# Performance work log

Hardware: AMD Instinct MI355X
Metric: run time of the kernel (lower is better)

## Reference

```python
import jax, jax.numpy as jnp
import numpy as np

B, L, H = 2, 4096, 1024


def _rope_tables(seq_len, dim, base=10000.0):
    # standard RoPE cos/sin tables, rotate-half convention, shape [L, dim]
    inv_freq = 1.0 / (base ** (np.arange(0, dim, 2, dtype=np.float32) / dim))
    t = np.arange(seq_len, dtype=np.float32)
    freqs = np.outer(t, inv_freq)                      # [L, dim/2]
    emb = np.concatenate([freqs, freqs], axis=-1)      # [L, dim]
    return jnp.asarray(np.cos(emb)), jnp.asarray(np.sin(emb))


def setup_inputs() -> dict:
    key = jax.random.key(0)
    k1, k2 = jax.random.split(key)
    hidden_states = jax.random.normal(k1, (B, L, H), dtype=jnp.float32)
    # queries weight: normal with std = initializer_range / sqrt(2*num_layers*hidden)
    std = 0.02 / np.sqrt(2.0 * 24 * H)
    W_q = jax.random.normal(k2, (H, H), dtype=jnp.float32) * std
    cos, sin = _rope_tables(L, H)
    return {"hidden_states": hidden_states, "W_q": W_q, "cos": cos, "sin": sin}


def _rotate_half(x):
    x1, x2 = jnp.split(x, 2, axis=-1)
    return jnp.concatenate([-x2, x1], axis=-1)


def reference(hidden_states, W_q, cos, sin):
    # dropout with p=0.0 (eval) -> identity
    h = hidden_states * cos[None, :, :] + _rotate_half(hidden_states) * sin[None, :, :]  # RoPE, [B,L,H]
    q = jnp.einsum('blh,oh->blo', h, W_q)          # F.linear(h, W_q), [B,L,H]
    pre_attn = jnp.einsum('blh,bmh->blm', q, h)    # Q @ K^T (no softmax), [B,L,L]
    attention = jnp.einsum('blm,bmh->blh', pre_attn, h)  # scores @ V, [B,L,H]
    return attention
```

## Files before the change

### kernel.cpp

```cpp
#include <hip/hip_runtime.h>
#include <hip/hip_bf16.h>
#include <stdint.h>

#define BB 2
#define LL 4096
#define HH 1024
#define GBK 32

typedef __bf16 bf16;
typedef __bf16 bf16x4 __attribute__((ext_vector_type(4)));
typedef __bf16 bf16x8 __attribute__((ext_vector_type(8)));
typedef float  f32x4  __attribute__((ext_vector_type(4)));

__device__ __forceinline__ void async_cp16(const bf16* g, const bf16* l)
{
    typedef const uint32_t __attribute__((address_space(1)))* gp_t;
    typedef uint32_t __attribute__((address_space(3)))* lp_t;
    __builtin_amdgcn_global_load_lds((gp_t)(uintptr_t)g, (lp_t)(uintptr_t)l, 16, 0, 0);
}

__device__ __forceinline__ uint32_t pack_bf16(float lo, float hi)
{
    union { bf16 b; unsigned short u; } a, c;
    a.b = (bf16)lo; c.b = (bf16)hi;
    return (uint32_t)a.u | ((uint32_t)c.u << 16);
}

__global__ __launch_bounds__(256) void prep_kernel(
    const float* __restrict__ x, const float* __restrict__ cs,
    const float* __restrict__ sn, const float* __restrict__ Wq,
    bf16* __restrict__ h, bf16* __restrict__ hT, bf16* __restrict__ Wb)
{
    const int id = blockIdx.x;
    if (id >= 1024) {
        const long base = (long)(id - 1024) * 4096 + (long)threadIdx.x * 16;
#pragma unroll
        for (int j = 0; j < 4; ++j) {
            const float4 v = *(const float4*)(Wq + base + j * 4);
            bf16x4 o;
            o[0] = (bf16)v.x; o[1] = (bf16)v.y; o[2] = (bf16)v.z; o[3] = (bf16)v.w;
            *(bf16x4*)(Wb + base + j * 4) = o;
        }
        return;
    }
    __shared__ uint32_t lds[2][64][36];
    const int b  = id >> 9;
    const int v  = id & 511;
    const int r0 = (v >> 3) * 64;
    const int c0 = (v & 7) * 64;
    const int t  = threadIdx.x;
    const int c8 = t & 7;
    const int rr = t >> 3;
    const int ca = c0 + c8 * 8;
    const long xrow0 = ((long)b * LL + r0 + 2 * rr) * HH;
    const long crow0 = (long)(r0 + 2 * rr) * HH;

    float oA[2][8], oB[2][8];
#pragma unroll
    for (int rw = 0; rw < 2; ++rw) {
        const long xr = xrow0 + (long)rw * HH;
        const long cr = crow0 + (long)rw * HH;
        float xA[8], xB[8], cA[8], sA[8];
        *(float4*)&xA[0] = *(const float4*)(x + xr + ca);
        *(float4*)&xA[4] = *(const float4*)(x + xr + ca + 4);
        *(float4*)&xB[0] = *(const float4*)(x + xr + ca + 512);
        *(float4*)&xB[4] = *(const float4*)(x + xr + ca + 516);
        *(float4*)&cA[0] = *(const float4*)(cs + cr + ca);
        *(float4*)&cA[4] = *(const float4*)(cs + cr + ca + 4);
        *(float4*)&sA[0] = *(const float4*)(sn + cr + ca);
        *(float4*)&sA[4] = *(const float4*)(sn + cr + ca + 4);
#pragma unroll
        for (int j = 0; j < 8; ++j) {
            oA[rw][j] = xA[j] * cA[j] - xB[j] * sA[j];
            oB[rw][j] = xB[j] * cA[j] + xA[j] * sA[j];
        }
        bf16x8 hA, hB;
#pragma unroll
        for (int j = 0; j < 8; ++j) { hA[j] = (bf16)oA[rw][j]; hB[j] = (bf16)oB[rw][j]; }
        *(bf16x8*)(h + xr + ca)       = hA;
        *(bf16x8*)(h + xr + ca + 512) = hB;
    }
#pragma unroll
    for (int j = 0; j < 8; ++j) {
        lds[0][c8 * 8 + j][rr] = pack_bf16(oA[0][j], oA[1][j]);
        lds[1][c8 * 8 + j][rr] = pack_bf16(oB[0][j], oB[1][j]);
    }
    __syncthreads();

    const int cc = t >> 2;
    const int q  = t & 3;
#pragma unroll
    for (int s = 0; s < 2; ++s) {
        const int hrow = (s ? c0 + 512 : c0) + cc;
        bf16* po = hT + (long)b * HH * LL + (long)hrow * LL + r0 + q * 16;
        const uint4 w0 = *(const uint4*)&lds[s][cc][q * 8];
        const uint4 w1 = *(const uint4*)&lds[s][cc][q * 8 + 4];
        *(uint4*)(po)     = w0;
        *(uint4*)(po + 8) = w1;
    }
}

__global__ __launch_bounds__(128) void rope_kernel(
    const float* __restrict__ x, const float* __restrict__ cs,
    const float* __restrict__ sn, bf16* __restrict__ h)
{
    const int l = blockIdx.x;
    const int b = blockIdx.y;
    const int i = threadIdx.x * 4;
    const long xb = ((long)b * LL + l) * HH;
    const long cb = (long)l * HH;
    const float4 x1 = *(const float4*)(x + xb + i);
    const float4 x2 = *(const float4*)(x + xb + i + HH / 2);
    const float4 c1 = *(const float4*)(cs + cb + i);
    const float4 c2 = *(const float4*)(cs + cb + i + HH / 2);
    const float4 s1 = *(const float4*)(sn + cb + i);
    const float4 s2 = *(const float4*)(sn + cb + i + HH / 2);
    bf16x4 o1, o2;
    o1[0] = (bf16)(x1.x * c1.x - x2.x * s1.x);
    o1[1] = (bf16)(x1.y * c1.y - x2.y * s1.y);
    o1[2] = (bf16)(x1.z * c1.z - x2.z * s1.z);
    o1[3] = (bf16)(x1.w * c1.w - x2.w * s1.w);
    o2[0] = (bf16)(x2.x * c2.x + x1.x * s2.x);
    o2[1] = (bf16)(x2.y * c2.y + x1.y * s2.y);
    o2[2] = (bf16)(x2.z * c2.z + x1.z * s2.z);
    o2[3] = (bf16)(x2.w * c2.w + x1.w * s2.w);
    *(bf16x4*)(h + xb + i)          = o1;
    *(bf16x4*)(h + xb + i + HH / 2) = o2;
}

__global__ __launch_bounds__(256) void transpose_bf16_64(
    const bf16* __restrict__ in, bf16* __restrict__ out, const int R, const int C)
{
    __shared__ uint32_t lds[64][36];
    const long zoff = (long)blockIdx.z * R * C;
    const int r0 = blockIdx.x * 64;
    const int c0 = blockIdx.y * 64;
    const int t  = threadIdx.x;
    const int c8 = t & 7;
    const int rr = t >> 3;
    const bf16* p0 = in + zoff + (long)(r0 + 2 * rr) * C + c0 + c8 * 8;
    const uint4 ra = *(const uint4*)p0;
    const uint4 rb = *(const uint4*)(p0 + C);
    const uint32_t av[4] = {ra.x, ra.y, ra.z, ra.w};
    const uint32_t bv[4] = {rb.x, rb.y, rb.z, rb.w};
#pragma unroll
    for (int j = 0; j < 4; ++j) {
        const uint32_t alo = av[j] & 0xffffu, ahi = av[j] >> 16;
        const uint32_t blo = bv[j] & 0xffffu, bhi = bv[j] >> 16;
        lds[c8 * 8 + 2 * j    ][rr] = alo | (blo << 16);
        lds[c8 * 8 + 2 * j + 1][rr] = ahi | (bhi << 16);
    }
    __syncthreads();
    const int c = t >> 2;
    const int q = t & 3;
    const uint4 w0 = *(const uint4*)&lds[c][q * 8];
    const uint4 w1 = *(const uint4*)&lds[c][q * 8 + 4];
    bf16* po = out + zoff + (long)(c0 + c) * R + r0 + q * 16;
    *(uint4*)(po)     = w0;
    *(uint4*)(po + 8) = w1;
}

__global__ __launch_bounds__(256) void cast_wq(
    const float* __restrict__ Wq, bf16* __restrict__ Wb)
{
    const long idx = ((long)blockIdx.x * 256 + threadIdx.x) * 4;
    const float4 v = *(const float4*)(Wq + idx);
    bf16x4 o;
    o[0] = (bf16)v.x; o[1] = (bf16)v.y; o[2] = (bf16)v.z; o[3] = (bf16)v.w;
    *(bf16x4*)(Wb + idx) = o;
}

#define GEMM_SHARED()                                                          \
    __shared__ __align__(16) bf16 As_[2][128][32];                             \
    __shared__ __align__(16) bf16 Bs_[2][128][32];

#define GEMM_PREFETCH(KOFF, BUF)                                               \
    do {                                                                       \
        async_cp16(Ag + (KOFF),           &As_[BUF][0][0] + woff0);            \
        async_cp16(Ag + (KOFF) + 64L * K, &As_[BUF][0][0] + woff1);            \
        async_cp16(Bg + (KOFF),           &Bs_[BUF][0][0] + woff0);            \
        async_cp16(Bg + (KOFF) + 64L * K, &Bs_[BUF][0][0] + woff1);            \
    } while (0)

#define GEMM_BODY(M0, N0, KBASE, KEND, DST, DT, LDN)                           \
    {                                                                          \
        const int tid  = threadIdx.x;                                          \
        const int lane = tid & 63;                                             \
        const int wave = tid >> 6;                                             \
        const int wm = (wave & 1) * 64;                                        \
        const int wn = (wave >> 1) * 64;                                       \
        const int fr = lane & 15;                                              \
        const int fq = lane >> 4;                                              \
        const int srow = tid >> 2;                                             \
        const int scol = (tid & 3) * 8;                                        \
        const int woff0 = wave * 512;                                          \
        const int woff1 = 2048 + wave * 512;                                   \
        const bf16* Ag = Ab + (long)((M0) + srow) * K + scol;                  \
        const bf16* Bg = Bb + (long)((N0) + srow) * K + scol;                  \
        const f32x4 vzero = {0.f, 0.f, 0.f, 0.f};                              \
        f32x4 acc[4][4];                                                       \
        _Pragma("unroll") for (int i = 0; i < 4; ++i)                          \
            _Pragma("unroll") for (int j = 0; j < 4; ++j) acc[i][j] = vzero;   \
        GEMM_PREFETCH(KBASE, 0);                                               \
        int buf = 0;                                                           \
        for (int k0 = (KBASE); k0 < (KEND); k0 += GBK, buf ^= 1) {             \
            __syncthreads();                                                   \
            if (k0 + GBK < (KEND)) GEMM_PREFETCH(k0 + GBK, buf ^ 1);           \
            bf16x8 af[4], bfv[4];                                              \
            _Pragma("unroll") for (int i = 0; i < 4; ++i)                      \
                af[i]  = *(const bf16x8*)&As_[buf][wm + i * 16 + fr][fq * 8];  \
            _Pragma("unroll") for (int j = 0; j < 4; ++j)                      \
                bfv[j] = *(const bf16x8*)&Bs_[buf][wn + j * 16 + fr][fq * 8];  \
            _Pragma("unroll") for (int i = 0; i < 4; ++i)                      \
                _Pragma("unroll") for (int j = 0; j < 4; ++j)                  \
                    acc[i][j] = __builtin_amdgcn_mfma_f32_16x16x32_bf16(       \
                        af[i], bfv[j], acc[i][j], 0, 0, 0);                    \
        }                                                                      \
        _Pragma("unroll") for (int i = 0; i < 4; ++i) {                        \
            _Pragma("unroll") for (int r = 0; r < 4; ++r) {                    \
                const int row = (M0) + wm + i * 16 + fq * 4 + r;               \
                _Pragma("unroll") for (int j = 0; j < 4; ++j) {                \
                    const int col = (N0) + wn + j * 16 + fr;                   \
                    (DST)[(long)row * (LDN) + col] = (DT)acc[i][j][r];         \
                }                                                              \
            }                                                                  \
        }                                                                      \
    }

template <typename OUT_T>
__global__ __launch_bounds__(256) void gemm_bt(
    const bf16* __restrict__ A, const bf16* __restrict__ B, OUT_T* __restrict__ C,
    const int M, const int N, const int K,
    const long sA, const long sB, const long sC)
{
    GEMM_SHARED();
    const bf16* Ab = A + blockIdx.z * sA;
    const bf16* Bb = B + blockIdx.z * sB;
    OUT_T*      Cb = C + blockIdx.z * sC;
    const int m0 = blockIdx.x * 128;
    const int n0 = blockIdx.y * 128;
    GEMM_BODY(m0, n0, 0, K, Cb, OUT_T, N);
}

#define E_STAGE_A(KT, PART, BUF)                                               \
  do {                                                                         \
    const int kk0_ = kbase + (KT) * 64;                                        \
    _Pragma("unroll") for (int qq_ = 0; qq_ < 2; ++qq_) {                      \
      const int ch_  = qq_ * 512 + tid;                                        \
      const int sl_  = ch_ >> 3;                                               \
      const int cc_  = (ch_ & 7) ^ (sl_ & 7);                                  \
      const int row_ = (sl_ & 63) + (PART) * 64 + ((sl_ >> 6) << 7);           \
      async_cp16(Ab + (long)(m0 + row_) * K + kk0_ + cc_ * 8,                  \
                 &As[BUF][PART][0][0] + (qq_ * 512 + (tid & 448)) * 8);        \
    }                                                                          \
  } while (0)

#define E_STAGE_B(KT, PART, BUF)                                               \
  do {                                                                         \
    const int kk0_ = kbase + (KT) * 64;                                        \
    _Pragma("unroll") for (int qq_ = 0; qq_ < 2; ++qq_) {                      \
      const int ch_  = qq_ * 512 + tid;                                        \
      const int sl_  = ch_ >> 3;                                               \
      const int cc_  = (ch_ & 7) ^ (sl_ & 7);                                  \
      const int row_ = (sl_ & 31) + (PART) * 32 + ((sl_ >> 5) << 6);           \
      async_cp16(Bb + (long)(n0 + row_) * K + kk0_ + cc_ * 8,                  \
                 &Bs[BUF][PART][0][0] + (qq_ * 512 + (tid & 448)) * 8);        \
    }                                                                          \
  } while (0)

#define E_STAGE_B2(KT, PART, BUF)                                              \
  do {                                                                         \
    const int kk0_ = kbase + (KT) * 64;                                        \
    const int sl_  = tid >> 3;                                                 \
    const int cc_  = (tid & 7) ^ (sl_ & 7);                                    \
    const int row_ = (sl_ & 15) + (PART) * 16 + ((sl_ >> 4) << 5);             \
    async_cp16(Bb + (long)(n0 + row_) * K + kk0_ + cc_ * 8,                    \
               &Bs2[BUF][PART][0][0] + (tid & 448) * 8);                       \
  } while (0)

#define E_LOAD_A(BUF, IG)                                                      \
  do {                                                                         \
    const bf16* Ap_ = &As[BUF][IG][0][0] + (wr * 64 + fr) * 64;                \
    _Pragma("unroll") for (int ii_ = 0; ii_ < 4; ++ii_)                        \
      _Pragma("unroll") for (int kk_ = 0; kk_ < 2; ++kk_)                      \
        af[ii_][kk_] = *(const bf16x8*)(Ap_ + ii_ * 1024 +                     \
                        (((kk_ * 4 + fq) ^ fr7) * 8));                         \
  } while (0)

#define E_LOAD_Bv(BUF, JP, DSTV)                                               \
  do {                                                                         \
    const bf16* Bp_ = &Bs[BUF][JP][0][0] + (wc * 32 + fr) * 64;                \
    _Pragma("unroll") for (int jj_ = 0; jj_ < 2; ++jj_)                        \
      _Pragma("unroll") for (int kk_ = 0; kk_ < 2; ++kk_)                      \
        DSTV[jj_][kk_] = *(const bf16x8*)(Bp_ + jj_ * 1024 +                   \
                        (((kk_ * 4 + fq) ^ fr7) * 8));                         \
  } while (0)

#define E_LOAD_B2(BUF, JG, DSTV)                                               \
  do {                                                                         \
    const bf16* Bp_ = &Bs2[BUF][JG][0][0] + (wc * 16 + fr) * 64;               \
    _Pragma("unroll") for (int kk_ = 0; kk_ < 2; ++kk_)                        \
      DSTV[kk_] = *(const bf16x8*)(Bp_ + (((kk_ * 4 + fq) ^ fr7) * 8));        \
  } while (0)

#define E_MMA(IG, JG, BV)                                                      \
  do {                                                                         \
    __builtin_amdgcn_s_setprio(1);                                             \
    _Pragma("unroll") for (int ii_ = 0; ii_ < 4; ++ii_)                        \
      _Pragma("unroll") for (int jj_ = 0; jj_ < 2; ++jj_)                      \
        _Pragma("unroll") for (int kk_ = 0; kk_ < 2; ++kk_)                    \
          acc[(IG) * 4 + ii_][(JG) * 2 + jj_] =                                \
              __builtin_amdgcn_mfma_f32_16x16x32_bf16(                         \
                  af[ii_][kk_], BV[jj_][kk_],                                  \
                  acc[(IG) * 4 + ii_][(JG) * 2 + jj_], 0, 0, 0);               \
    __builtin_amdgcn_s_setprio(0);                                             \
  } while (0)

#define E_MMA2(IG, JG, BV)                                                     \
  do {                                                                         \
    __builtin_amdgcn_s_setprio(1);                                             \
    _Pragma("unroll") for (int ii_ = 0; ii_ < 4; ++ii_)                        \
      _Pragma("unroll") for (int kk_ = 0; kk_ < 2; ++kk_)                      \
        acc2[(IG) * 4 + ii_][JG] =                                             \
            __builtin_amdgcn_mfma_f32_16x16x32_bf16(                           \
                af[ii_][kk_], BV[kk_], acc2[(IG) * 4 + ii_][JG], 0, 0, 0);     \
    __builtin_amdgcn_s_setprio(0);                                             \
  } while (0)

#define E_BAR()   __builtin_amdgcn_s_barrier()
#define E_LGKM0() do { asm volatile("s_waitcnt lgkmcnt(0)" ::: "memory");      \
                       __builtin_amdgcn_sched_barrier(0); } while (0)
#define E_VM(N)   asm volatile("s_waitcnt vmcnt(" #N ")" ::: "memory")

#define E_COMMON_IDX()                                                         \
  const int tid  = threadIdx.x;                                                \
  const int lane = tid & 63;                                                   \
  const int wv   = tid >> 6;                                                   \
  const int wr   = wv >> 2;                                                    \
  const int wc   = wv & 3;                                                     \
  const int fr   = lane & 15;                                                  \
  const int fq   = lane >> 4;                                                  \
  const int fr7  = fr & 7;                                                     \
  (void)lane;

__global__ __launch_bounds__(512, 2) void gemm8_Gq(
    const bf16* __restrict__ hT, const bf16* __restrict__ Wb,
    const bf16* __restrict__ h, bf16* __restrict__ P, bf16* __restrict__ q)
{
    __shared__ __align__(16) bf16 As[2][2][128][64];
    __shared__ __align__(16) bf16 Bs[2][2][128][64];
    E_COMMON_IDX();
    bf16x8 af[4][2], bfv0[2][2], bfv1[2][2];
    f32x4 acc[8][4];
#pragma unroll
    for (int i_ = 0; i_ < 8; ++i_)
#pragma unroll
        for (int j_ = 0; j_ < 4; ++j_) acc[i_][j_] = (f32x4){0.f, 0.f, 0.f, 0.f};

    const int bid = blockIdx.x;
    const int id  = (bid & 7) * 32 + (bid >> 3);
    const bf16* Ab; const bf16* Bb;
    int K, kbase, m0, n0;
    bf16* Cb;
    if (id < 128) {
        m0 = (id >> 2) * 256;
        n0 = (id & 3) * 256;
        Ab = h; Bb = Wb; K = HH; kbase = 0;
        Cb = q;
    } else {
        const int u  = id - 128;
        const int pl = u >> 4;
        const int zb = pl >> 2;
        const int zs = pl & 3;
        const int tl = u & 15;
        m0 = (tl & 3) * 256;
        n0 = (tl >> 2) * 256;
        Ab = hT + (long)zb * HH * LL; Bb = Ab;
        K  = LL; kbase = zs * (LL / 4);
        Cb = P + (long)pl * HH * HH;
    }

    E_STAGE_A(0, 0, 0); E_STAGE_B(0, 1, 0); E_STAGE_A(0, 1, 0);
    E_STAGE_B(0, 0, 0);
    E_STAGE_A(1, 0, 1); E_STAGE_B(1, 1, 1); E_STAGE_A(1, 1, 1);
    E_VM(6); E_BAR();
    int t_ = 0;
#pragma unroll 1
    for (; t_ + 3 < 16; t_ += 2) {
         E_LOAD_A(0, 0); E_LOAD_Bv(0, 0, bfv0); E_STAGE_B(t_ + 1, 0, 1);
                 E_BAR(); E_LGKM0(); E_MMA(0, 0, bfv0); E_BAR();
         E_LOAD_Bv(0, 1, bfv1); E_STAGE_A(t_ + 2, 0, 0);
                 E_BAR(); E_LGKM0(); E_MMA(0, 1, bfv1); E_BAR();
         E_LOAD_A(0, 1); E_STAGE_B(t_ + 2, 1, 0);
                 E_BAR(); E_LGKM0(); E_MMA(1, 1, bfv1); E_BAR();
         E_STAGE_A(t_ + 2, 1, 0);
                 E_MMA(1, 0, bfv0); E_VM(6); E_BAR();
         E_LOAD_A(1, 0); E_LOAD_Bv(1, 0, bfv0); E_STAGE_B(t_ + 2, 0, 0);
                 E_BAR(); E_LGKM0(); E_MMA(0, 0, bfv0); E_BAR();
         E_LOAD_Bv(1, 1, bfv1); E_STAGE_A(t_ + 3, 0, 1);
                 E_BAR(); E_LGKM0(); E_MMA(0, 1, bfv1); E_BAR();
         E_LOAD_A(1, 1); E_STAGE_B(t_ + 3, 1, 1);
                 E_BAR(); E_LGKM0(); E_MMA(1, 1, bfv1); E_BAR();
         E_STAGE_A(t_ + 3, 1, 1);
                 E_MMA(1, 0, bfv0); E_VM(6); E_BAR();
    }
    E_LOAD_A(0, 0); E_LOAD_Bv(0, 0, bfv0); E_STAGE_B(t_ + 1, 0, 1);
    E_BAR(); E_LGKM0(); E_MMA(0, 0, bfv0); E_BAR();
    E_LOAD_Bv(0, 1, bfv1); E_BAR(); E_LGKM0(); E_MMA(0, 1, bfv1); E_BAR();
    E_LOAD_A(0, 1); E_BAR(); E_LGKM0(); E_MMA(1, 1, bfv1); E_BAR();
    E_MMA(1, 0, bfv0); E_VM(0); E_BAR();
    E_LOAD_A(1, 0); E_LOAD_Bv(1, 0, bfv0); E_BAR(); E_LGKM0(); E_MMA(0, 0, bfv0); E_BAR();
    E_LOAD_Bv(1, 1, bfv1); E_BAR(); E_LGKM0(); E_MMA(0, 1, bfv1); E_BAR();
    E_LOAD_A(1, 1); E_BAR(); E_LGKM0(); E_MMA(1, 1, bfv1); E_BAR();
    E_MMA(1, 0, bfv0);

#pragma unroll
    for (int gi = 0; gi < 8; ++gi)
#pragma unroll
        for (int r = 0; r < 4; ++r) {
            const int row = m0 + wr * 128 + gi * 16 + fq * 4 + r;
#pragma unroll
            for (int gj = 0; gj < 4; ++gj)
                Cb[(long)row * HH + n0 + wc * 64 + gj * 16 + fr] = (bf16)acc[gi][gj][r];
        }
}

__global__ __launch_bounds__(512, 2) void gemm8_qG(
    const bf16* __restrict__ qm, const bf16* __restrict__ G, float* __restrict__ out)
{
    __shared__ __align__(16) bf16 As[2][2][128][64];
    __shared__ __align__(16) bf16 Bs2[2][2][64][64];
    E_COMMON_IDX();
    bf16x8 af[4][2], bw0[2], bw1[2];
    f32x4 acc2[8][2];
#pragma unroll
    for (int i_ = 0; i_ < 8; ++i_)
#pragma unroll
        for (int j_ = 0; j_ < 2; ++j_) acc2[i_][j_] = (f32x4){0.f, 0.f, 0.f, 0.f};

    const int bid = blockIdx.x;
    const int id  = (bid & 7) * 32 + (bid >> 3);
    const int mb  = id >> 3;
    const int b   = mb >> 4;
    const int m0  = (mb & 15) * 256;
    const int n0  = (id & 7) * 128;
    const bf16* Ab = qm + (long)b * LL * HH;
    const bf16* Bb = G + (long)b * HH * HH;
    const int K = HH, kbase = 0;
    float* outb = out + (long)b * LL * HH;

    E_STAGE_A(0, 0, 0); E_STAGE_B2(0, 1, 0); E_STAGE_A(0, 1, 0);
    E_STAGE_B2(0, 0, 0);
    E_STAGE_A(1, 0, 1); E_STAGE_B2(1, 1, 1); E_STAGE_A(1, 1, 1);
    E_VM(5); E_BAR();
    int t_ = 0;
#pragma unroll 1
    for (; t_ + 3 < 16; t_ += 2) {
         E_LOAD_A(0, 0); E_LOAD_B2(0, 0, bw0); E_STAGE_B2(t_ + 1, 0, 1);
                 E_BAR(); E_LGKM0(); E_MMA2(0, 0, bw0); E_BAR();
         E_LOAD_B2(0, 1, bw1); E_STAGE_A(t_ + 2, 0, 0);
                 E_BAR(); E_LGKM0(); E_MMA2(0, 1, bw1); E_BAR();
         E_LOAD_A(0, 1); E_STAGE_B2(t_ + 2, 1, 0);
                 E_BAR(); E_LGKM0(); E_MMA2(1, 1, bw1); E_BAR();
         E_STAGE_A(t_ + 2, 1, 0);
                 E_MMA2(1, 0, bw0); E_VM(5); E_BAR();
         E_LOAD_A(1, 0); E_LOAD_B2(1, 0, bw0); E_STAGE_B2(t_ + 2, 0, 0);
                 E_BAR(); E_LGKM0(); E_MMA2(0, 0, bw0); E_BAR();
         E_LOAD_B2(1, 1, bw1); E_STAGE_A(t_ + 3, 0, 1);
                 E_BAR(); E_LGKM0(); E_MMA2(0, 1, bw1); E_BAR();
         E_LOAD_A(1, 1); E_STAGE_B2(t_ + 3, 1, 1);
                 E_BAR(); E_LGKM0(); E_MMA2(1, 1, bw1); E_BAR();
         E_STAGE_A(t_ + 3, 1, 1);
                 E_MMA2(1, 0, bw0); E_VM(5); E_BAR();
    }
    E_LOAD_A(0, 0); E_LOAD_B2(0, 0, bw0); E_STAGE_B2(t_ + 1, 0, 1);
    E_BAR(); E_LGKM0(); E_MMA2(0, 0, bw0); E_BAR();
    E_LOAD_B2(0, 1, bw1); E_BAR(); E_LGKM0(); E_MMA2(0, 1, bw1); E_BAR();
    E_LOAD_A(0, 1); E_BAR(); E_LGKM0(); E_MMA2(1, 1, bw1); E_BAR();
    E_MMA2(1, 0, bw0); E_VM(0); E_BAR();
    E_LOAD_A(1, 0); E_LOAD_B2(1, 0, bw0); E_BAR(); E_LGKM0(); E_MMA2(0, 0, bw0); E_BAR();
    E_LOAD_B2(1, 1, bw1); E_BAR(); E_LGKM0(); E_MMA2(0, 1, bw1); E_BAR();
    E_LOAD_A(1, 1); E_BAR(); E_LGKM0(); E_MMA2(1, 1, bw1); E_BAR();
    E_MMA2(1, 0, bw0);

#pragma unroll
    for (int gi = 0; gi < 8; ++gi)
#pragma unroll
        for (int r = 0; r < 4; ++r) {
            const int row = m0 + wr * 128 + gi * 16 + fq * 4 + r;
#pragma unroll
            for (int gj = 0; gj < 2; ++gj)
                outb[(long)row * HH + n0 + wc * 32 + gj * 16 + fr] = acc2[gi][gj][r];
        }
}

__global__ __launch_bounds__(256) void reduce_splits(
    const bf16* __restrict__ P, bf16* __restrict__ out, const int npb, const int S)
{
    const int b = blockIdx.y;
    const long r = ((long)blockIdx.x * 256 + threadIdx.x) * 8;
    const bf16* base = P + (long)b * S * npb + r;
    float a[8];
    {
        const bf16x8 v = *(const bf16x8*)(base);
#pragma unroll
        for (int j = 0; j < 8; ++j) a[j] = (float)v[j];
    }
    for (int s = 1; s < S; ++s) {
        const bf16x8 v = *(const bf16x8*)(base + (long)s * npb);
#pragma unroll
        for (int j = 0; j < 8; ++j) a[j] += (float)v[j];
    }
    bf16x8 o;
#pragma unroll
    for (int j = 0; j < 8; ++j) o[j] = (bf16)a[j];
    *(bf16x8*)(out + (long)b * npb + r) = o;
}

extern "C" void kernel_launch(void* const* d_in, const int* in_sizes, int n_in,
                              void* d_out, int out_size, void* d_ws, size_t ws_size,
                              hipStream_t stream)
{
    const float* x  = (const float*)d_in[0];
    const float* Wq = (const float*)d_in[1];
    const float* cs = (const float*)d_in[2];
    const float* sn = (const float*)d_in[3];
    float* out = (float*)d_out;
    char* ws = (char*)d_ws;

    bf16*  h  = (bf16*)(ws);
    bf16*  hT = (bf16*)(ws + 16u * 1024 * 1024);
    bf16*  Wb = (bf16*)(ws + 32u * 1024 * 1024);
    bf16*  G  = (bf16*)(ws + 34u * 1024 * 1024);
    bf16*  P  = (bf16*)(ws + 38u * 1024 * 1024);

    const bool big_ws = ws_size >= (size_t)90 * 1024 * 1024;
    bf16* q = big_ws ? (bf16*)(ws + 70u * 1024 * 1024)
                     : (bf16*)(ws + 54u * 1024 * 1024);

    if (big_ws) {
        prep_kernel<<<dim3(1280), 256, 0, stream>>>(x, cs, sn, Wq, h, hT, Wb);
        gemm8_Gq<<<dim3(256), 512, 0, stream>>>(hT, Wb, h, P, q);
        reduce_splits<<<dim3(HH * HH / 2048, BB), 256, 0, stream>>>(P, G, HH * HH, 4);
        gemm8_qG<<<dim3(256), 512, 0, stream>>>(q, G, out);
    } else {
        rope_kernel<<<dim3(LL, BB), 128, 0, stream>>>(x, cs, sn, h);
        transpose_bf16_64<<<dim3(LL / 64, HH / 64, BB), 256, 0, stream>>>(h, hT, LL, HH);
        cast_wq<<<dim3(HH * HH / 1024), 256, 0, stream>>>(Wq, Wb);
        gemm_bt<bf16><<<dim3(HH / 128, HH / 128, BB), 256, 0, stream>>>(
            hT, hT, G, HH, HH, LL, (long)HH * LL, (long)HH * LL, (long)HH * HH);
        gemm_bt<bf16><<<dim3(LL / 128, HH / 128, BB), 256, 0, stream>>>(
            h, Wb, q, LL, HH, HH, (long)LL * HH, 0L, (long)LL * HH);
        gemm_bt<float><<<dim3(LL / 128, HH / 128, BB), 256, 0, stream>>>(
            q, G, out, LL, HH, HH, (long)LL * HH, (long)HH * HH, (long)LL * HH);
    }
}
```

Before: 173.4 us.

## Fuse split-K reduction into Gram GEMM using atomic ticket counters

After: 297.0 us. +71.3%, slower.

```diff
diff --git a/kernel.cpp b/kernel.cpp
--- a/kernel.cpp
+++ b/kernel.cpp
@@ -29,10 +29,12 @@
 __global__ __launch_bounds__(256) void prep_kernel(
     const float* __restrict__ x, const float* __restrict__ cs,
     const float* __restrict__ sn, const float* __restrict__ Wq,
-    bf16* __restrict__ h, bf16* __restrict__ hT, bf16* __restrict__ Wb)
+    bf16* __restrict__ h, bf16* __restrict__ hT, bf16* __restrict__ Wb,
+    unsigned* __restrict__ tickets)
 {
     const int id = blockIdx.x;
     if (id >= 1024) {
+        if (id == 1024 && threadIdx.x < 32) tickets[threadIdx.x] = 0u;
         const long base = (long)(id - 1024) * 4096 + (long)threadIdx.x * 16;
 #pragma unroll
         for (int j = 0; j < 4; ++j) {
@@ -345,10 +347,12 @@
 
 __global__ __launch_bounds__(512, 2) void gemm8_Gq(
     const bf16* __restrict__ hT, const bf16* __restrict__ Wb,
-    const bf16* __restrict__ h, bf16* __restrict__ P, bf16* __restrict__ q)
+    const bf16* __restrict__ h, bf16* __restrict__ P, bf16* __restrict__ q,
+    bf16* __restrict__ G, unsigned* __restrict__ tickets)
 {
     __shared__ __align__(16) bf16 As[2][2][128][64];
     __shared__ __align__(16) bf16 Bs[2][2][128][64];
+    __shared__ int lastFlag;
     E_COMMON_IDX();
     bf16x8 af[4][2], bfv0[2][2], bfv1[2][2];
     f32x4 acc[8][4];
@@ -362,6 +366,7 @@
     const bf16* Ab; const bf16* Bb;
     int K, kbase, m0, n0;
     bf16* Cb;
+    int gtick = -1, gzb = 0;
     if (id < 128) {
         m0 = (id >> 2) * 256;
         n0 = (id & 3) * 256;
@@ -378,6 +383,7 @@
         Ab = hT + (long)zb * HH * LL; Bb = Ab;
         K  = LL; kbase = zs * (LL / 4);
         Cb = P + (long)pl * HH * HH;
+        gtick = zb * 16 + tl; gzb = zb;
     }
 
     E_STAGE_A(0, 0, 0); E_STAGE_B(0, 1, 0); E_STAGE_A(0, 1, 0);
@@ -423,6 +429,38 @@
             for (int gj = 0; gj < 4; ++gj)
                 Cb[(long)row * HH + n0 + wc * 64 + gj * 16 + fr] = (bf16)acc[gi][gj][r];
         }
+
+    if (gtick >= 0) {
+        __threadfence();
+        if (tid == 0) {
+            const unsigned prev = atomicAdd(&tickets[gtick], 1u);
+            lastFlag = (prev == 3u);
+        }
+        __syncthreads();
+        if (lastFlag) {
+            __threadfence();
+            const bf16* P0 = P + (long)(gzb * 4) * HH * HH;
+            bf16* Gb = G + (long)gzb * HH * HH;
+            const int row  = tid >> 1;
+            const long base = (long)(m0 + row) * HH + n0 + (tid & 1) * 128;
+#pragma unroll
+            for (int v = 0; v < 16; ++v) {
+                const long off = base + v * 8;
+                float a[8];
+                const bf16x8 v0 = *(const bf16x8*)(P0 + off);
+                const bf16x8 v1 = *(const bf16x8*)(P0 + off + (long)1 * HH * HH);
+                const bf16x8 v2 = *(const bf16x8*)(P0 + off + (long)2 * HH * HH);
+                const bf16x8 v3 = *(const bf16x8*)(P0 + off + (long)3 * HH * HH);
+#pragma unroll
+                for (int j = 0; j < 8; ++j)
+                    a[j] = (float)v0[j] + (float)v1[j] + (float)v2[j] + (float)v3[j];
+                bf16x8 o;
+#pragma unroll
+                for (int j = 0; j < 8; ++j) o[j] = (bf16)a[j];
+                *(bf16x8*)(Gb + off) = o;
+            }
+        }
+    }
 }
 
 __global__ __launch_bounds__(512, 2) void gemm8_qG(
@@ -494,29 +532,6 @@
         }
 }
 
-__global__ __launch_bounds__(256) void reduce_splits(
-    const bf16* __restrict__ P, bf16* __restrict__ out, const int npb, const int S)
-{
-    const int b = blockIdx.y;
-    const long r = ((long)blockIdx.x * 256 + threadIdx.x) * 8;
-    const bf16* base = P + (long)b * S * npb + r;
-    float a[8];
-    {
-        const bf16x8 v = *(const bf16x8*)(base);
-#pragma unroll
-        for (int j = 0; j < 8; ++j) a[j] = (float)v[j];
-    }
-    for (int s = 1; s < S; ++s) {
-        const bf16x8 v = *(const bf16x8*)(base + (long)s * npb);
-#pragma unroll
-        for (int j = 0; j < 8; ++j) a[j] += (float)v[j];
-    }
-    bf16x8 o;
-#pragma unroll
-    for (int j = 0; j < 8; ++j) o[j] = (bf16)a[j];
-    *(bf16x8*)(out + (long)b * npb + r) = o;
-}
-
 extern "C" void kernel_launch(void* const* d_in, const int* in_sizes, int n_in,
                               void* d_out, int out_size, void* d_ws, size_t ws_size,
                               hipStream_t stream)
@@ -537,11 +552,11 @@
     const bool big_ws = ws_size >= (size_t)90 * 1024 * 1024;
     bf16* q = big_ws ? (bf16*)(ws + 70u * 1024 * 1024)
                      : (bf16*)(ws + 54u * 1024 * 1024);
+    unsigned* tickets = (unsigned*)(ws + 87u * 1024 * 1024);
 
     if (big_ws) {
-        prep_kernel<<<dim3(1280), 256, 0, stream>>>(x, cs, sn, Wq, h, hT, Wb);
-        gemm8_Gq<<<dim3(256), 512, 0, stream>>>(hT, Wb, h, P, q);
-        reduce_splits<<<dim3(HH * HH / 2048, BB), 256, 0, stream>>>(P, G, HH * HH, 4);
+        prep_kernel<<<dim3(1280), 256, 0, stream>>>(x, cs, sn, Wq, h, hT, Wb, tickets);
+        gemm8_Gq<<<dim3(256), 512, 0, stream>>>(hT, Wb, h, P, q, G, tickets);
         gemm8_qG<<<dim3(256), 512, 0, stream>>>(q, G, out);
     } else {
         rope_kernel<<<dim3(LL, BB), 128, 0, stream>>>(x, cs, sn, h);
```
